# Optimization experiments

Measured on AMD Instinct MI355X. Metric: run time of the kernel, lower is better.

Reference implementation:

```python
import jax, jax.numpy as jnp
import numpy as np

B, S_IMG, S_TXT = 2, 2048, 256
DIM, H, D = 1024, 16, 64
EPS = 1e-6


def _rmsnorm(x, w):
    x32 = x.astype(jnp.float32)
    rms = jnp.sqrt(jnp.mean(x32 * x32, axis=-1, keepdims=True) + EPS)
    return (x32 / rms * w.astype(jnp.float32)).astype(x.dtype)


def _heads(x):  # [B,S,DIM] -> [B,H,S,D]
    b, s, _ = x.shape
    return x.reshape(b, s, H, D).transpose(0, 2, 1, 3)


def setup_inputs() -> dict:
    key = jax.random.key(0)
    ks = jax.random.split(key, 20)
    lin = lambda k: (jax.random.normal(k, (DIM, DIM), jnp.float32) * 0.02,
                     jnp.zeros((DIM,), jnp.float32))
    wq, bq = lin(ks[0]); wk, bk = lin(ks[1]); wv, bv = lin(ks[2])
    waq, baq = lin(ks[3]); wak, bak = lin(ks[4]); wav, bav = lin(ks[5])
    wout, bout = lin(ks[6]); waout, baout = lin(ks[7])
    return {
        "img_hidden": jax.random.normal(ks[8], (B, S_IMG, DIM), jnp.float32),
        "txt_hidden": jax.random.normal(ks[9], (B, S_TXT, DIM), jnp.float32),
        "wq": wq, "bq": bq, "wk": wk, "bk": bk, "wv": wv, "bv": bv,
        "waq": waq, "baq": baq, "wak": wak, "bak": bak, "wav": wav, "bav": bav,
        "wout": wout, "bout": bout, "waout": waout, "baout": baout,
        "gq": jnp.ones((D,), jnp.float32), "gk": jnp.ones((D,), jnp.float32),
        "gaq": jnp.ones((D,), jnp.float32), "gak": jnp.ones((D,), jnp.float32),
    }


def reference(img_hidden, txt_hidden, wq, bq, wk, bk, wv, bv,
              waq, baq, wak, bak, wav, bav, wout, bout, waout, baout,
              gq, gk, gaq, gak):
    batch = img_hidden.shape[0]
    # joint QKV projections (torch Linear: x @ W.T + b)
    q = _heads(img_hidden @ wq.T + bq)
    k = _heads(img_hidden @ wk.T + bk)
    v = _heads(img_hidden @ wv.T + bv)
    aq = _heads(txt_hidden @ waq.T + baq)
    ak = _heads(txt_hidden @ wak.T + bak)
    av = _heads(txt_hidden @ wav.T + bav)
    # per-head RMSNorm on Q/K
    q, k = _rmsnorm(q, gq), _rmsnorm(k, gk)
    aq, ak = _rmsnorm(aq, gaq), _rmsnorm(ak, gak)
    # concat streams along sequence: [B,H,S_img+S_txt,D]
    fq = jnp.concatenate([q, aq], axis=2)
    fk = jnp.concatenate([k, ak], axis=2)
    fv = jnp.concatenate([v, av], axis=2)
    scale = 1.0 / jnp.sqrt(jnp.float32(D))
    attn = jnp.einsum('bhqd,bhkd->bhqk', fq, fk) * scale
    attn = jax.nn.softmax(attn, axis=-1)
    out = jnp.einsum('bhqk,bhkd->bhqd', attn, fv)
    out = out.transpose(0, 2, 1, 3)  # [B,S,H,D]
    s_img = q.shape[2]
    img_out = out[:, :s_img].reshape(batch, s_img, -1)
    txt_out = out[:, s_img:].reshape(batch, aq.shape[2], -1)
    img_out = img_out @ wout.T + bout
    txt_out = txt_out @ waout.T + baout
    return (img_out, txt_out)
```

## Files before the change

### kernel.cpp

```cpp
#include <hip/hip_runtime.h>
#include <stdint.h>

#define BATCH 2
#define SIMG 2048
#define STXT 256
#define STOT 2304
#define DIM 1024
#define NH 16
#define HD 64

typedef unsigned short u16;
typedef __attribute__((ext_vector_type(8))) short bf16x8;
typedef __attribute__((ext_vector_type(4))) float f32x4;
typedef __attribute__((ext_vector_type(2))) uint32_t u32x2;

__device__ __forceinline__ u16 f2bf(float f) {
  union { float f; uint32_t u; } v; v.f = f;
  uint32_t r = (v.u + 0x7FFFu + ((v.u >> 16) & 1u)) >> 16;
  return (u16)r;
}
__device__ __forceinline__ float bf2f(u16 h) {
  union { uint32_t u; float f; } v; v.u = ((uint32_t)h) << 16; return v.f;
}

__device__ __forceinline__ void async_load16(const u16* g, u16* l) {
  __builtin_amdgcn_global_load_lds(
      (const __attribute__((address_space(1))) uint32_t*)g,
      (__attribute__((address_space(3))) uint32_t*)l, 16, 0, 0);
}

__device__ __forceinline__ bf16x8 cvt8(const float* p) {
  const f32x4 a = *(const f32x4*)p;
  const f32x4 b = *(const f32x4*)(p + 4);
  union { bf16x8 v; u16 s[8]; } r;
  r.s[0] = f2bf(a[0]); r.s[1] = f2bf(a[1]); r.s[2] = f2bf(a[2]); r.s[3] = f2bf(a[3]);
  r.s[4] = f2bf(b[0]); r.s[5] = f2bf(b[1]); r.s[6] = f2bf(b[2]); r.s[7] = f2bf(b[3]);
  return r.v;
}

__device__ __forceinline__ float gain_at(const u16* g, int d) {
  if (g[0] == 0) return ((const float*)g)[d];
  return bf2f(g[d]);
}

__global__ __launch_bounds__(256)
void cvt_all(const float* s0, const float* s1, const float* s2, const float* s3,
             const float* s4, const float* s5, const float* s6, const float* s7,
             const float* s8, const float* s9,
             u16* d0, u16* d1, u16* d2, u16* d3, u16* d4,
             u16* d5, u16* d6, u16* d7, u16* d8, u16* d9)
{
  const int z = blockIdx.z;
  const float* srcs[10] = {s0,s1,s2,s3,s4,s5,s6,s7,s8,s9};
  u16* dsts[10] = {d0,d1,d2,d3,d4,d5,d6,d7,d8,d9};
  const int ns[10] = {BATCH*SIMG*DIM, BATCH*STXT*DIM, DIM*DIM, DIM*DIM, DIM*DIM,
                      DIM*DIM, DIM*DIM, DIM*DIM, DIM*DIM, DIM*DIM};
  const long i = ((long)blockIdx.x * 256 + threadIdx.x) * 8;
  if (i >= ns[z]) return;
  *(bf16x8*)(dsts[z] + i) = cvt8(srcs[z] + i);
}

template<int MODE>
__global__ __launch_bounds__(256)
void gemm_bt(const u16* __restrict__ Ai, const u16* __restrict__ At,
             const u16* __restrict__ Wi0, const u16* __restrict__ Wi1, const u16* __restrict__ Wi2,
             const u16* __restrict__ Wt0, const u16* __restrict__ Wt1, const u16* __restrict__ Wt2,
             const float* __restrict__ bi0, const float* __restrict__ bi1, const float* __restrict__ bi2,
             const float* __restrict__ bt0, const float* __restrict__ bt1, const float* __restrict__ bt2,
             void* __restrict__ Di0, void* __restrict__ Di1, void* __restrict__ Di2,
             void* __restrict__ Dt0, void* __restrict__ Dt1, void* __restrict__ Dt2,
             const u16* __restrict__ gi0, const u16* __restrict__ gi1,
             const u16* __restrict__ gt0, const u16* __restrict__ gt1,
             int ysplit)
{
  const int z = blockIdx.z;
  const bool txt = (int)blockIdx.y >= ysplit;
  const int yy = txt ? ((int)blockIdx.y - ysplit) : (int)blockIdx.y;

  const u16* A = txt ? At : Ai;
  const u16* W      = txt ? ((z == 0) ? Wt0 : ((z == 1) ? Wt1 : Wt2))
                          : ((z == 0) ? Wi0 : ((z == 1) ? Wi1 : Wi2));
  const float* bias = txt ? ((z == 0) ? bt0 : ((z == 1) ? bt1 : bt2))
                          : ((z == 0) ? bi0 : ((z == 1) ? bi1 : bi2));
  void* Dst         = txt ? ((z == 0) ? Dt0 : ((z == 1) ? Dt1 : Dt2))
                          : ((z == 0) ? Di0 : ((z == 1) ? Di1 : Di2));

  const int slog = txt ? 8 : 11;
  const int smask = (1 << slog) - 1;
  const int batch_rows = (MODE == 0) ? (txt ? STXT : SIMG) : STOT;
  const int src_off    = (MODE == 0) ? 0 : (txt ? SIMG : 0);
  const int dst_off    = (MODE == 0) ? (txt ? SIMG : 0) : 0;

  const int m0 = yy * 128;
  const int n0 = blockIdx.x * 128;
  const int tid = threadIdx.x;
  const int lane = tid & 63;
  const int w = tid >> 6;
  const int wm = w >> 1, wn = w & 1;
  const int l15 = lane & 15, quad = lane >> 4;

  __shared__ __attribute__((aligned(16))) u16 As[128 * 32];
  __shared__ __attribute__((aligned(16))) u16 Bs[128 * 32];

  const int srow = tid >> 2;
  const int scol = (tid & 3) * 8;

  long aoff0, aoff1;
  {
    int m = m0 + srow;
    aoff0 = ((long)(m >> slog) * batch_rows + src_off + (m & smask)) * DIM + scol;
    m = m0 + 64 + srow;
    aoff1 = ((long)(m >> slog) * batch_rows + src_off + (m & smask)) * DIM + scol;
  }
  const u16* wp0 = W + (long)(n0 + srow) * DIM + scol;
  const u16* wp1 = W + (long)(n0 + 64 + srow) * DIM + scol;
  u16* as0 = As + tid * 8;
  u16* as1 = As + 2048 + tid * 8;
  u16* bs0 = Bs + tid * 8;
  u16* bs1 = Bs + 2048 + tid * 8;

  const f32x4 fzero = {0.f, 0.f, 0.f, 0.f};
  f32x4 acc[4][4];
  #pragma unroll
  for (int i = 0; i < 4; ++i)
    #pragma unroll
    for (int j = 0; j < 4; ++j) acc[i][j] = fzero;

  for (int kt = 0; kt < DIM; kt += 32) {
    __syncthreads();
    async_load16(A + aoff0 + kt, as0);
    async_load16(A + aoff1 + kt, as1);
    async_load16(wp0 + kt, bs0);
    async_load16(wp1 + kt, bs1);
    __syncthreads();

    bf16x8 af[4], bfg[4];
    #pragma unroll
    for (int mt = 0; mt < 4; ++mt)
      af[mt] = *(const bf16x8*)(As + (wm * 64 + mt * 16 + l15) * 32 + quad * 8);
    #pragma unroll
    for (int nt = 0; nt < 4; ++nt)
      bfg[nt] = *(const bf16x8*)(Bs + (wn * 64 + nt * 16 + l15) * 32 + quad * 8);
    #pragma unroll
    for (int mt = 0; mt < 4; ++mt)
      #pragma unroll
      for (int nt = 0; nt < 4; ++nt)
        acc[mt][nt] = __builtin_amdgcn_mfma_f32_16x16x32_bf16(af[mt], bfg[nt], acc[mt][nt], 0, 0, 0);
  }

  if (MODE == 0 && z != 2) {
    const u16* gsel = txt ? ((z == 0) ? gt0 : gt1) : ((z == 0) ? gi0 : gi1);
    float gv[4];
    #pragma unroll
    for (int nt = 0; nt < 4; ++nt) gv[nt] = gain_at(gsel, nt * 16 + l15);
    #pragma unroll
    for (int mt = 0; mt < 4; ++mt) {
      float vals[4][4];
      #pragma unroll
      for (int nt = 0; nt < 4; ++nt) {
        const float bb = bias[n0 + wn * 64 + nt * 16 + l15];
        #pragma unroll
        for (int r = 0; r < 4; ++r) vals[nt][r] = acc[mt][nt][r] + bb;
      }
      #pragma unroll
      for (int r = 0; r < 4; ++r) {
        float ss = vals[0][r] * vals[0][r] + vals[1][r] * vals[1][r]
                 + vals[2][r] * vals[2][r] + vals[3][r] * vals[3][r];
        #pragma unroll
        for (int d = 1; d < 16; d <<= 1) ss += __shfl_xor(ss, d, 64);
        const float scn = rsqrtf(ss * (1.0f / 64.0f) + 1e-6f);
        const int grow = m0 + wm * 64 + mt * 16 + quad * 4 + r;
        const int b = grow >> slog;
        const int sl = grow & smask;
        #pragma unroll
        for (int nt = 0; nt < 4; ++nt) {
          const int gcol = n0 + wn * 64 + nt * 16 + l15;
          const int h = gcol >> 6, d2 = gcol & 63;
          const long idx = (((long)(b * NH + h)) * STOT + dst_off + sl) * HD + d2;
          ((u16*)Dst)[idx] = f2bf(vals[nt][r] * scn * gv[nt]);
        }
      }
    }
  } else {
    #pragma unroll
    for (int mt = 0; mt < 4; ++mt) {
      #pragma unroll
      for (int nt = 0; nt < 4; ++nt) {
        const int gcol = n0 + wn * 64 + nt * 16 + l15;
        const float bb = bias[gcol];
        const f32x4 v = acc[mt][nt];
        #pragma unroll
        for (int r = 0; r < 4; ++r) {
          const int grow = m0 + wm * 64 + mt * 16 + quad * 4 + r;
          const float val = v[r] + bb;
          if (MODE == 0) {
            const int b = grow >> slog;
            const int sl = grow & smask;
            const int h = gcol >> 6, d = gcol & 63;
            const long idx = (((long)(b * NH + h)) * HD + d) * STOT + dst_off + sl;
            ((u16*)Dst)[idx] = f2bf(val);
          } else {
            ((float*)Dst)[(long)grow * DIM + gcol] = val;
          }
        }
      }
    }
  }
}

__global__ __launch_bounds__(256)
void flash_attn_split(const u16* __restrict__ fq, const u16* __restrict__ fk,
                      const u16* __restrict__ fvT,
                      u16* __restrict__ p0, u16* __restrict__ p1,
                      float* __restrict__ l0, float* __restrict__ l1)
{
  const int qt = blockIdx.x;
  const int bh = blockIdx.y;
  const int z = blockIdx.z;
  u16* pout = z ? p1 : p0;
  float* lout = z ? l1 : l0;
  const int it0 = z * (STOT / 128);

  const int tid = threadIdx.x;
  const int lane = tid & 63;
  const int w = tid >> 6;
  const int l15 = lane & 15, quad = lane >> 4;
  const int x7 = l15 & 7;
  const long base = (long)bh * STOT * HD;
  const int b = bh >> 4, h = bh & 15;

  __shared__ __attribute__((aligned(16))) u16 Ks[64 * 64];
  __shared__ __attribute__((aligned(16))) u16 Vt[64 * 64];
  __shared__ __attribute__((aligned(16))) u16 Ps[64 * 72];

  bf16x8 aq[2];
  #pragma unroll
  for (int ks = 0; ks < 2; ++ks)
    aq[ks] = *(const bf16x8*)(fq + base +
        (long)(qt * 64 + w * 16 + l15) * 64 + ks * 32 + quad * 8);

  const f32x4 fzero = {0.f, 0.f, 0.f, 0.f};
  f32x4 Oc[4];
  float lsum = 0.f;
  #pragma unroll
  for (int nt = 0; nt < 4; ++nt) Oc[nt] = fzero;

  const float C1 = 0.18033688011112042f;
  const float C8 = 11.541560327111707f;

  const int srow = tid >> 3;
  const int sseg = (tid & 7) ^ (srow & 7);
  const int sr2 = srow + 32;
  u16* const pwr = Ps + (w * 16 + l15) * 72 + quad * 4;

  for (int it = it0; it < it0 + STOT / 128; ++it) {
    __syncthreads();
    const u16* ksrc = fk + base + (long)it * 64 * 64;
    async_load16(ksrc + srow * 64 + sseg * 8, Ks + tid * 8);
    async_load16(ksrc + sr2 * 64 + sseg * 8, Ks + 2048 + tid * 8);
    const u16* vsrc = fvT + base + (long)it * 64;
    async_load16(vsrc + (long)srow * STOT + sseg * 8, Vt + tid * 8);
    async_load16(vsrc + (long)sr2 * STOT + sseg * 8, Vt + 2048 + tid * 8);
    __syncthreads();

    f32x4 sc[4];
    #pragma unroll
    for (int nt = 0; nt < 4; ++nt) sc[nt] = fzero;
    #pragma unroll
    for (int ks = 0; ks < 2; ++ks) {
      bf16x8 bk[4];
      #pragma unroll
      for (int nt = 0; nt < 4; ++nt)
        bk[nt] = *(const bf16x8*)(Ks + (nt * 16 + l15) * 64 + (((ks * 4 + quad) ^ x7) * 8));
      #pragma unroll
      for (int nt = 0; nt < 4; ++nt)
        sc[nt] = __builtin_amdgcn_mfma_f32_16x16x32_bf16(bk[nt], aq[ks], sc[nt], 0, 0, 0);
    }

    #pragma unroll
    for (int nt = 0; nt < 4; ++nt) {
      const uint32_t u0 = __float_as_uint(exp2f(sc[nt][0] * C1 - C8));
      const uint32_t u1 = __float_as_uint(exp2f(sc[nt][1] * C1 - C8));
      const uint32_t u2 = __float_as_uint(exp2f(sc[nt][2] * C1 - C8));
      const uint32_t u3 = __float_as_uint(exp2f(sc[nt][3] * C1 - C8));
      u32x2 pk;
      pk[0] = (u0 >> 16) | (u1 & 0xFFFF0000u);
      pk[1] = (u2 >> 16) | (u3 & 0xFFFF0000u);
      *(u32x2*)(pwr + nt * 16) = pk;
      lsum += __uint_as_float(u0 & 0xFFFF0000u) + __uint_as_float(u1 & 0xFFFF0000u)
            + __uint_as_float(u2 & 0xFFFF0000u) + __uint_as_float(u3 & 0xFFFF0000u);
    }

    #pragma unroll
    for (int ks = 0; ks < 2; ++ks) {
      const bf16x8 ap = *(const bf16x8*)(Ps + (w * 16 + l15) * 72 + ks * 32 + quad * 8);
      bf16x8 bv[4];
      #pragma unroll
      for (int nt = 0; nt < 4; ++nt)
        bv[nt] = *(const bf16x8*)(Vt + (nt * 16 + l15) * 64 + (((ks * 4 + quad) ^ x7) * 8));
      #pragma unroll
      for (int nt = 0; nt < 4; ++nt)
        Oc[nt] = __builtin_amdgcn_mfma_f32_16x16x32_bf16(ap, bv[nt], Oc[nt], 0, 0, 0);
    }
  }

  float ls = lsum;
  ls += __shfl_xor(ls, 16, 64);
  ls += __shfl_xor(ls, 32, 64);
  if (quad == 0)
    lout[(long)bh * STOT + qt * 64 + w * 16 + l15] = ls;
  const float inv = 1.0f / ls;
  float inv4[4];
  #pragma unroll
  for (int r = 0; r < 4; ++r)
    inv4[r] = __shfl(inv, quad * 4 + r, 64);

  #pragma unroll
  for (int nt = 0; nt < 4; ++nt) {
    const int d = nt * 16 + l15;
    #pragma unroll
    for (int r = 0; r < 4; ++r) {
      const int q = qt * 64 + w * 16 + quad * 4 + r;
      pout[(((long)b * STOT + q) * NH + h) * HD + d] = f2bf(Oc[nt][r]);
    }
  }
}

__global__ __launch_bounds__(256)
void attn_combine(const u16* __restrict__ p1, const float* __restrict__ l0,
                  const float* __restrict__ l1, u16* __restrict__ p0io)
{
  const long i = ((long)blockIdx.x * 256 + threadIdx.x) * 8;
  const long rem = i >> 6;
  const int h = (int)(rem & 15);
  const long bq = rem >> 4;
  const int b = bq >= STOT;
  const int q = (int)(bq - (long)b * STOT);
  const long li = ((long)(b * NH + h)) * STOT + q;
  const float inv = 1.0f / (l0[li] + l1[li]);
  union { bf16x8 v; u16 s[8]; } a, c, o;
  a.v = *(const bf16x8*)(p0io + i);
  c.v = *(const bf16x8*)(p1 + i);
  #pragma unroll
  for (int j = 0; j < 8; ++j)
    o.s[j] = f2bf((bf2f(a.s[j]) + bf2f(c.s[j])) * inv);
  *(bf16x8*)(p0io + i) = o.v;
}

extern "C" void kernel_launch(void* const* d_in, const int* in_sizes, int n_in,
                              void* d_out, int out_size, void* d_ws, size_t ws_size,
                              hipStream_t stream)
{
  int iImg = 0, iTxt = 1;
  if (in_sizes[0] < in_sizes[1]) { iImg = 1; iTxt = 0; }
  const float* img  = (const float*)d_in[iImg];
  const float* txt  = (const float*)d_in[iTxt];
  const float* wq   = (const float*)d_in[2];
  const float* bq   = (const float*)d_in[3];
  const float* wk   = (const float*)d_in[4];
  const float* bk   = (const float*)d_in[5];
  const float* wv   = (const float*)d_in[6];
  const float* bv   = (const float*)d_in[7];
  const float* waq  = (const float*)d_in[8];
  const float* baq  = (const float*)d_in[9];
  const float* wak  = (const float*)d_in[10];
  const float* bak  = (const float*)d_in[11];
  const float* wav  = (const float*)d_in[12];
  const float* bav  = (const float*)d_in[13];
  const float* wout = (const float*)d_in[14];
  const float* bout = (const float*)d_in[15];
  const float* waout= (const float*)d_in[16];
  const float* baout= (const float*)d_in[17];
  const u16* gq   = (const u16*)d_in[18];
  const u16* gk   = (const u16*)d_in[19];
  const u16* gaq  = (const u16*)d_in[20];
  const u16* gak  = (const u16*)d_in[21];

  const long NE = (long)BATCH * NH * STOT * HD;
  const long NIMG = (long)BATCH * SIMG * DIM;
  const long NW = (long)DIM * DIM;

  u16* fq  = (u16*)d_ws;
  u16* fk  = fq + NE;
  u16* fvT = fk + NE;
  u16* imgb = fvT + NE;
  u16* txtb = imgb + NIMG;
  u16* aob  = imgb;
  u16* woutb  = imgb + NE;
  u16* waoutb = woutb + NW;
  float* lsum0 = (float*)(waoutb + NW);
  float* lsum1 = lsum0 + (long)BATCH * NH * STOT;
  u16* qw = (u16*)d_out;
  u16* wqb = qw, *wkb = qw + NW, *wvb = qw + 2*NW;
  u16* waqb = qw + 3*NW, *wakb = qw + 4*NW, *wavb = qw + 5*NW;
  u16* p1 = (u16*)d_out;
  float* out = (float*)d_out;
  float* outt = out + (long)BATCH * SIMG * DIM;

  const dim3 blk(256, 1, 1);

  hipLaunchKernelGGL(cvt_all, dim3((int)(NIMG / 2048), 1, 10), blk, 0, stream,
                     img, txt, wq, wk, wv, waq, wak, wav, wout, waout,
                     imgb, txtb, wqb, wkb, wvb, waqb, wakb, wavb, woutb, waoutb);
  hipLaunchKernelGGL((gemm_bt<0>), dim3(8, 36, 3), blk, 0, stream,
                     imgb, txtb, wqb, wkb, wvb, waqb, wakb, wavb,
                     bq, bk, bv, baq, bak, bav,
                     fq, fk, fvT, fq, fk, fvT,
                     gq, gk, gaq, gak, 32);
  hipLaunchKernelGGL(flash_attn_split, dim3(STOT / 64, BATCH * NH, 2), blk, 0, stream,
                     fq, fk, fvT, aob, p1, lsum0, lsum1);
  hipLaunchKernelGGL(attn_combine, dim3((int)(NE / 2048)), blk, 0, stream,
                     p1, lsum0, lsum1, aob);
  hipLaunchKernelGGL((gemm_bt<1>), dim3(8, 36, 1), blk, 0, stream,
                     aob, aob, woutb, woutb, woutb, waoutb, waoutb, waoutb,
                     bout, bout, bout, baout, baout, baout,
                     out, out, out, outt, outt, outt,
                     nullptr, nullptr, nullptr, nullptr, 32);
}
```

Measured before the change: 303.3 us.

## Swizzle GEMM LDS tiles and transpose MFMA operands for V-transposed store

XORs the 16-byte chunk index in the A/B shared-memory tiles with row bits, on both the async load side and the fragment read side, to cut LDS bank conflicts. For the V projection, which is stored transposed, the MFMA operands are swapped so each lane holds consecutive sequence rows. The store to the transposed V buffer can then be better coalesced along the sequence dimension. It also removes an unused reciprocal/shuffle block in the attention kernel and adds a dedicated epilogue branch.

```diff
diff --git a/kernel.cpp b/kernel.cpp
--- a/kernel.cpp
+++ b/kernel.cpp
@@ -98,12 +98,14 @@
   const int w = tid >> 6;
   const int wm = w >> 1, wn = w & 1;
   const int l15 = lane & 15, quad = lane >> 4;
+  const int rsw = (l15 >> 1) & 3;
 
   __shared__ __attribute__((aligned(16))) u16 As[128 * 32];
   __shared__ __attribute__((aligned(16))) u16 Bs[128 * 32];
 
   const int srow = tid >> 2;
-  const int scol = (tid & 3) * 8;
+  const int schunk = (tid & 3) ^ ((srow >> 1) & 3);
+  const int scol = schunk * 8;
 
   long aoff0, aoff1;
   {
@@ -126,6 +128,8 @@
     #pragma unroll
     for (int j = 0; j < 4; ++j) acc[i][j] = fzero;
 
+  const bool vswap = (MODE == 0) && (z == 2);
+
   for (int kt = 0; kt < DIM; kt += 32) {
     __syncthreads();
     async_load16(A + aoff0 + kt, as0);
@@ -137,15 +141,23 @@
     bf16x8 af[4], bfg[4];
     #pragma unroll
     for (int mt = 0; mt < 4; ++mt)
-      af[mt] = *(const bf16x8*)(As + (wm * 64 + mt * 16 + l15) * 32 + quad * 8);
+      af[mt] = *(const bf16x8*)(As + (wm * 64 + mt * 16 + l15) * 32 + ((quad ^ rsw) * 8));
     #pragma unroll
     for (int nt = 0; nt < 4; ++nt)
-      bfg[nt] = *(const bf16x8*)(Bs + (wn * 64 + nt * 16 + l15) * 32 + quad * 8);
-    #pragma unroll
-    for (int mt = 0; mt < 4; ++mt)
-      #pragma unroll
-      for (int nt = 0; nt < 4; ++nt)
-        acc[mt][nt] = __builtin_amdgcn_mfma_f32_16x16x32_bf16(af[mt], bfg[nt], acc[mt][nt], 0, 0, 0);
+      bfg[nt] = *(const bf16x8*)(Bs + (wn * 64 + nt * 16 + l15) * 32 + ((quad ^ rsw) * 8));
+    if (vswap) {
+      #pragma unroll
+      for (int mt = 0; mt < 4; ++mt)
+        #pragma unroll
+        for (int nt = 0; nt < 4; ++nt)
+          acc[mt][nt] = __builtin_amdgcn_mfma_f32_16x16x32_bf16(bfg[nt], af[mt], acc[mt][nt], 0, 0, 0);
+    } else {
+      #pragma unroll
+      for (int mt = 0; mt < 4; ++mt)
+        #pragma unroll
+        for (int nt = 0; nt < 4; ++nt)
+          acc[mt][nt] = __builtin_amdgcn_mfma_f32_16x16x32_bf16(af[mt], bfg[nt], acc[mt][nt], 0, 0, 0);
+    }
   }
 
   if (MODE == 0 && z != 2) {
@@ -181,6 +193,29 @@
         }
       }
     }
+  } else if (MODE == 0) {
+    float bv[4][4];
+    #pragma unroll
+    for (int nt = 0; nt < 4; ++nt)
+      #pragma unroll
+      for (int r = 0; r < 4; ++r)
+        bv[nt][r] = bias[n0 + wn * 64 + nt * 16 + quad * 4 + r];
+    #pragma unroll
+    for (int mt = 0; mt < 4; ++mt) {
+      const int grow = m0 + wm * 64 + mt * 16 + l15;
+      const int b = grow >> slog;
+      const int sl = grow & smask;
+      #pragma unroll
+      for (int nt = 0; nt < 4; ++nt) {
+        #pragma unroll
+        for (int r = 0; r < 4; ++r) {
+          const int gcol = n0 + wn * 64 + nt * 16 + quad * 4 + r;
+          const int h = gcol >> 6, d = gcol & 63;
+          const long idx = (((long)(b * NH + h)) * HD + d) * STOT + dst_off + sl;
+          ((u16*)Dst)[idx] = f2bf(acc[mt][nt][r] + bv[nt][r]);
+        }
+      }
+    }
   } else {
     #pragma unroll
     for (int mt = 0; mt < 4; ++mt) {
@@ -192,16 +227,7 @@
         #pragma unroll
         for (int r = 0; r < 4; ++r) {
           const int grow = m0 + wm * 64 + mt * 16 + quad * 4 + r;
-          const float val = v[r] + bb;
-          if (MODE == 0) {
-            const int b = grow >> slog;
-            const int sl = grow & smask;
-            const int h = gcol >> 6, d = gcol & 63;
-            const long idx = (((long)(b * NH + h)) * HD + d) * STOT + dst_off + sl;
-            ((u16*)Dst)[idx] = f2bf(val);
-          } else {
-            ((float*)Dst)[(long)grow * DIM + gcol] = val;
-          }
+          ((float*)Dst)[(long)grow * DIM + gcol] = v[r] + bb;
         }
       }
     }
@@ -309,11 +335,6 @@
   ls += __shfl_xor(ls, 32, 64);
   if (quad == 0)
     lout[(long)bh * STOT + qt * 64 + w * 16 + l15] = ls;
-  const float inv = 1.0f / ls;
-  float inv4[4];
-  #pragma unroll
-  for (int r = 0; r < 4; ++r)
-    inv4[r] = __shfl(inv, quad * 4 + r, 64);
 
   #pragma unroll
   for (int nt = 0; nt < 4; ++nt) {
```

After: 347.9 us. +14.7%, slower.
